# Kernel tuning notes

Hardware: AMD Instinct MI355X
Metric: run time of the kernel (lower is better)

## Reference

```python
import jax, jax.numpy as jnp
import numpy as np

TOP_K = 8
N_GROUPS = 8
TOP_K_GROUPS = 4
ROUTE_SCALE = 2.5


def setup_inputs() -> dict:
    key = jax.random.key(0)
    k1, k2, k3 = jax.random.split(key, 3)
    x = jax.random.normal(k1, (8192, 7168), dtype=jnp.float32)
    weight = jax.random.normal(k2, (256, 7168), dtype=jnp.float32) * 0.02
    bias = jax.random.normal(k3, (256,), dtype=jnp.float32) * 0.1
    return {"x": x, "weight": weight, "bias": bias}


def reference(x, weight, bias):
    n_tokens = x.shape[0]
    n_experts = weight.shape[0]
    # scores: [T, E]
    logits = jnp.einsum('td,ed->te', x, weight)
    scores = jax.nn.sigmoid(logits)
    original_scores = scores
    scores_b = scores + bias  # bias branch (dim == 7168)
    # group-limited routing
    sg = scores_b.reshape(n_tokens, N_GROUPS, n_experts // N_GROUPS)
    # bias is not None -> group score = sum of top-2 within group
    top2, _ = jax.lax.top_k(sg, 2)
    group_scores = top2.sum(axis=-1)  # [T, G]
    _, group_idx = jax.lax.top_k(group_scores, TOP_K_GROUPS)  # [T, Kg]
    keep = jnp.zeros((n_tokens, N_GROUPS), dtype=bool)
    keep = keep.at[jnp.arange(n_tokens)[:, None], group_idx].set(True)
    masked = jnp.where(keep[:, :, None], sg, -jnp.inf).reshape(n_tokens, n_experts)
    # global top-k over masked scores
    _, indices = jax.lax.top_k(masked, TOP_K)  # [T, K]
    weights = jnp.take_along_axis(original_scores, indices, axis=1)
    weights = weights / weights.sum(axis=-1, keepdims=True)  # sigmoid normalization
    weights = weights * ROUTE_SCALE
    return weights.astype(x.dtype), indices
```

## Files before the change

### kernel.cpp

```cpp
#include <hip/hip_runtime.h>
#include <math.h>

#define T_TOKENS 8192
#define NEXP 256
#define DIM 7168
#define NSPLIT 4
#define KSPL (DIM / NSPLIT)
#define NITER (KSPL / 32)
#define NEG_INF (-3.0e38f)

typedef _Float16 f16;
typedef _Float16 f16x8 __attribute__((ext_vector_type(8)));
typedef __fp16 h16x2 __attribute__((ext_vector_type(2)));
typedef float f32x4 __attribute__((ext_vector_type(4)));
typedef float f32x16 __attribute__((ext_vector_type(16)));

#define AS1 __attribute__((address_space(1)))
#define AS3 __attribute__((address_space(3)))
typedef const AS1 f16x8* gf16x8p;

#define WTILED_BYTES (2 * NEXP * DIM * 2)
#define PART_OFF WTILED_BYTES
#define UNSCALE 5.9604644775390625e-8f
#define STG 8192

__global__ __launch_bounds__(256) void wconvert(const float* __restrict__ w,
                                                char* __restrict__ wt) {
    const int n = blockIdx.x * 256 + threadIdx.x;
    const int K8 = n % 896;
    const int e = n / 896;
    const f32x4 u0 = *(const f32x4*)(w + (size_t)e * DIM + K8 * 8);
    const f32x4 u1 = *(const f32x4*)(w + (size_t)e * DIM + K8 * 8 + 4);
    float c[8] = {u0[0]*4096.f, u0[1]*4096.f, u0[2]*4096.f, u0[3]*4096.f,
                  u1[0]*4096.f, u1[1]*4096.f, u1[2]*4096.f, u1[3]*4096.f};
    f16x8 h, g;
#pragma unroll
    for (int j = 0; j < 4; ++j) {
        h16x2 hp = __builtin_amdgcn_cvt_pkrtz(c[2*j], c[2*j+1]);
        float r0 = c[2*j]   - (float)hp[0];
        float r1 = c[2*j+1] - (float)hp[1];
        h16x2 gp = __builtin_amdgcn_cvt_pkrtz(r0, r1);
        h[2*j] = (f16)hp[0]; h[2*j+1] = (f16)hp[1];
        g[2*j] = (f16)gp[0]; g[2*j+1] = (f16)gp[1];
    }
    const int T = K8 >> 2;
    const int kk = (K8 >> 1) & 1;
    const int lhi = K8 & 1;
    const int ntg = e >> 5, l31 = e & 31;
    char* base = wt + (size_t)T * 32768 + ntg * 1024 + lhi * 512 + l31 * 16;
    *(f16x8*)(base + (kk * 2 + 0) * 8192) = h;
    *(f16x8*)(base + (kk * 2 + 1) * 8192) = g;
}

__global__ __launch_bounds__(512, 4) void gemm_fo(
    const float* __restrict__ x, const char* __restrict__ wt,
    float* __restrict__ part) {
    __shared__ char smem[3 * STG];
    const int tid = threadIdx.x;
    const int lane = tid & 63;
    const int wcn = tid >> 6;
    const int b = blockIdx.x;
    const int xcd = b & 7;
    const int bz = xcd >> 1;
    const int bm = (xcd & 1) * 64 + (b >> 3);
    const int l31 = lane & 31, lhi = lane >> 5;

    const char* xc = (const char*)x;

    const int mt_s = wcn >> 2, kk_s = (wcn >> 1) & 1, j_s = wcn & 1;
    const int aoff = ((bm * 64 + mt_s * 32 + l31) * DIM + bz * KSPL
                      + kk_s * 16 + lhi * 8 + j_s * 4) * 4;
    const int ldsA = wcn * 1024;

    const AS1 char* wq = (const AS1 char*)(wt + (size_t)bz * NITER * 32768
                                           + wcn * 1024 + lane * 16);

    f32x16 acc[2];
#pragma unroll
    for (int mt = 0; mt < 2; ++mt)
#pragma unroll
        for (int r = 0; r < 16; ++r) acc[mt][r] = 0.0f;

    f16x8 wA[2][2], wB[2][2];

#define LOAD_W(T, WDST)                                                         \
    {                                                                           \
        _Pragma("unroll")                                                       \
        for (int kk = 0; kk < 2; ++kk)                                          \
            _Pragma("unroll")                                                   \
            for (int p = 0; p < 2; ++p)                                         \
                WDST[kk][p] = *(gf16x8p)(wq + (size_t)(T) * 32768 + (kk * 2 + p) * 8192); \
    }

#define COMPUTE(CB, W)                                                          \
    {                                                                           \
        _Pragma("unroll")                                                       \
        for (int kk = 0; kk < 2; ++kk) {                                        \
            _Pragma("unroll")                                                   \
            for (int mt = 0; mt < 2; ++mt) {                                    \
                const f32x4 v0 = *(const f32x4*)(smem + (CB) + (mt * 4 + kk * 2 + 0) * 1024 + lane * 16); \
                const f32x4 v1 = *(const f32x4*)(smem + (CB) + (mt * 4 + kk * 2 + 1) * 1024 + lane * 16); \
                float c[8] = {v0[0]*4096.f, v0[1]*4096.f, v0[2]*4096.f, v0[3]*4096.f,\
                              v1[0]*4096.f, v1[1]*4096.f, v1[2]*4096.f, v1[3]*4096.f};\
                f16x8 a0, a1;                                                   \
                _Pragma("unroll")                                               \
                for (int j = 0; j < 4; ++j) {                                   \
                    h16x2 hp = __builtin_amdgcn_cvt_pkrtz(c[2*j], c[2*j+1]);    \
                    float r0 = c[2*j]   - (float)hp[0];                         \
                    float r1 = c[2*j+1] - (float)hp[1];                         \
                    h16x2 gp = __builtin_amdgcn_cvt_pkrtz(r0, r1);              \
                    a0[2*j] = (f16)hp[0]; a0[2*j+1] = (f16)hp[1];               \
                    a1[2*j] = (f16)gp[0]; a1[2*j+1] = (f16)gp[1];               \
                }                                                               \
                __builtin_amdgcn_s_setprio(1);                                  \
                acc[mt] = __builtin_amdgcn_mfma_f32_32x32x16_f16(a0, W[kk][0], acc[mt], 0, 0, 0); \
                acc[mt] = __builtin_amdgcn_mfma_f32_32x32x16_f16(a1, W[kk][0], acc[mt], 0, 0, 0); \
                acc[mt] = __builtin_amdgcn_mfma_f32_32x32x16_f16(a0, W[kk][1], acc[mt], 0, 0, 0); \
                acc[mt] = __builtin_amdgcn_mfma_f32_32x32x16_f16(a1, W[kk][1], acc[mt], 0, 0, 0); \
                __builtin_amdgcn_s_setprio(0);                                  \
            }                                                                   \
        }                                                                       \
    }

#define BODY(T, WCUR, WNXT)                                                     \
    {                                                                           \
        asm volatile("s_waitcnt vmcnt(1)" ::: "memory");                        \
        __builtin_amdgcn_sched_barrier(0);                                      \
        __builtin_amdgcn_s_barrier();    \
        const int tw = ((T) + 1 < NITER) ? (T) + 1 : 0;                         \
        LOAD_W(tw, WNXT);                                                       \
        const int ts = ((T) + 2 < NITER) ? (T) + 2 : 0;                         \
        __builtin_amdgcn_global_load_lds(                                       \
            (const AS1 void*)(xc + aoff + ts * 128),                            \
            (AS3 void*)(smem + sb + ldsA), 16, 0, 0);                           \
        COMPUTE(cb, WCUR);                                                      \
        cb = (cb == 2 * STG) ? 0 : cb + STG;                                    \
        sb = (sb == 2 * STG) ? 0 : sb + STG;                                    \
    }

    __builtin_amdgcn_global_load_lds((const AS1 void*)(xc + aoff),
                                     (AS3 void*)(smem + ldsA), 16, 0, 0);
    LOAD_W(0, wA);
    __builtin_amdgcn_global_load_lds((const AS1 void*)(xc + aoff + 128),
                                     (AS3 void*)(smem + STG + ldsA), 16, 0, 0);

    int cb = 0, sb = 2 * STG;
    for (int tt = 0; tt < NITER; tt += 2) {
        BODY(tt, wA, wB);
        BODY(tt + 1, wB, wA);
    }
#undef BODY
#undef COMPUTE
#undef LOAD_W

    float* P = part + (size_t)bz * T_TOKENS * NEXP;
    const int gcol = wcn * 32 + l31;
#pragma unroll
    for (int mt = 0; mt < 2; ++mt)
#pragma unroll
        for (int r = 0; r < 16; ++r) {
            const int row32 = (r & 3) + 8 * (r >> 2) + 4 * lhi;
            const int grow = bm * 64 + mt * 32 + row32;
            P[(size_t)grow * NEXP + gcol] = acc[mt][r];
        }
}

__global__ __launch_bounds__(256) void routing_kernel(const float* __restrict__ part,
                                                      const float* __restrict__ bias,
                                                      float* __restrict__ out) {
    const int lane = threadIdx.x & 63;
    const int t = blockIdx.x * 4 + (threadIdx.x >> 6);

    f32x4 z = {0.f, 0.f, 0.f, 0.f};
#pragma unroll
    for (int s = 0; s < NSPLIT; ++s) {
        const f32x4 v = *((const f32x4*)(part + ((size_t)s * T_TOKENS + t) * NEXP) + lane);
        z[0] += v[0]; z[1] += v[1]; z[2] += v[2]; z[3] += v[3];
    }
    const float s0 = 1.0f / (1.0f + expf(-z[0] * UNSCALE));
    const float s1 = 1.0f / (1.0f + expf(-z[1] * UNSCALE));
    const float s2 = 1.0f / (1.0f + expf(-z[2] * UNSCALE));
    const float s3 = 1.0f / (1.0f + expf(-z[3] * UNSCALE));
    const f32x4 bv = *((const f32x4*)bias + lane);
    float sb0 = s0 + bv[0], sb1 = s1 + bv[1], sb2 = s2 + bv[2], sb3 = s3 + bv[3];

    float m1, m2;
    m1 = sb0; m2 = NEG_INF;
    if (sb1 > m1) { m2 = m1; m1 = sb1; } else if (sb1 > m2) m2 = sb1;
    if (sb2 > m1) { m2 = m1; m1 = sb2; } else if (sb2 > m2) m2 = sb2;
    if (sb3 > m1) { m2 = m1; m1 = sb3; } else if (sb3 > m2) m2 = sb3;
#pragma unroll
    for (int off = 1; off < 8; off <<= 1) {
        const float om1 = __shfl_xor(m1, off);
        const float om2 = __shfl_xor(m2, off);
        const float hi = fmaxf(m1, om1);
        const float lo = fminf(m1, om1);
        m2 = fmaxf(lo, fmaxf(m2, om2));
        m1 = hi;
    }
    const float gs = m1 + m2;

    const float g0 = __shfl(gs, 0),  g1 = __shfl(gs, 8),  g2 = __shfl(gs, 16), g3 = __shfl(gs, 24);
    const float g4 = __shfl(gs, 32), g5 = __shfl(gs, 40), g6 = __shfl(gs, 48), g7 = __shfl(gs, 56);

    float t1 = NEG_INF, t2 = NEG_INF, t3 = NEG_INF, t4 = NEG_INF;
    int i1 = 0, i2 = 0, i3 = 0, i4 = 0;
#define INS4(v, gi)                                                         \
    {                                                                       \
        if (v > t1)      { t4=t3;i4=i3; t3=t2;i3=i2; t2=t1;i2=i1; t1=v;i1=gi; } \
        else if (v > t2) { t4=t3;i4=i3; t3=t2;i3=i2; t2=v;i2=gi; }          \
        else if (v > t3) { t4=t3;i4=i3; t3=v;i3=gi; }                       \
        else if (v > t4) { t4=v;i4=gi; }                                    \
    }
    INS4(g0, 0) INS4(g1, 1) INS4(g2, 2) INS4(g3, 3)
    INS4(g4, 4) INS4(g5, 5) INS4(g6, 6) INS4(g7, 7)
#undef INS4
    const int keepmask = (1 << i1) | (1 << i2) | (1 << i3) | (1 << i4);

    const int g = lane >> 3;
    if (!((keepmask >> g) & 1)) { sb0 = NEG_INF; sb1 = NEG_INF; sb2 = NEG_INF; sb3 = NEG_INF; }

    float wval[8];
    int wi[8];
    float wsum = 0.0f;
#pragma unroll
    for (int r = 0; r < 8; r++) {
        float bvv = sb0;
        int bii = (lane << 2);
        if (sb1 > bvv) { bvv = sb1; bii = (lane << 2) | 1; }
        if (sb2 > bvv) { bvv = sb2; bii = (lane << 2) | 2; }
        if (sb3 > bvv) { bvv = sb3; bii = (lane << 2) | 3; }
#pragma unroll
        for (int off = 1; off < 64; off <<= 1) {
            const float ov = __shfl_xor(bvv, off);
            const int oi = __shfl_xor(bii, off);
            if (ov > bvv || (ov == bvv && oi < bii)) { bvv = ov; bii = oi; }
        }
        const int sl = bii & 3;
        const float cand = (sl == 0) ? s0 : (sl == 1) ? s1 : (sl == 2) ? s2 : s3;
        const float ow = __shfl(cand, bii >> 2);
        wval[r] = ow;
        wi[r] = bii;
        wsum += ow;
        if ((bii >> 2) == lane) {
            if (sl == 0) sb0 = NEG_INF;
            else if (sl == 1) sb1 = NEG_INF;
            else if (sl == 2) sb2 = NEG_INF;
            else sb3 = NEG_INF;
        }
    }
    const float scale = 2.5f / wsum;
    if (lane == 0) {
        float* ow8 = out + (size_t)t * 8;
        float* oi8 = out + (size_t)T_TOKENS * 8 + (size_t)t * 8;
#pragma unroll
        for (int r = 0; r < 8; r++) {
            ow8[r] = wval[r] * scale;
            oi8[r] = (float)wi[r];
        }
    }
}

extern "C" void kernel_launch(void* const* d_in, const int* in_sizes, int n_in,
                              void* d_out, int out_size, void* d_ws, size_t ws_size,
                              hipStream_t stream) {
    const float* x = (const float*)d_in[0];
    const float* w = (const float*)d_in[1];
    const float* bias = (const float*)d_in[2];

    char* wt = (char*)d_ws;
    float* part = (float*)((char*)d_ws + PART_OFF);

    wconvert<<<NEXP * DIM / (256 * 8), 256, 0, stream>>>(w, wt);
    gemm_fo<<<512, 512, 0, stream>>>(x, wt, part);
    routing_kernel<<<T_TOKENS / 4, 256, 0, stream>>>(part, bias, (float*)d_out);
}
```

Measured before the change: 169.8 us.

## Stage weight tiles through LDS and split waves over M and N

```diff
diff --git a/kernel.cpp b/kernel.cpp
--- a/kernel.cpp
+++ b/kernel.cpp
@@ -17,12 +17,11 @@
 
 #define AS1 __attribute__((address_space(1)))
 #define AS3 __attribute__((address_space(3)))
-typedef const AS1 f16x8* gf16x8p;
 
 #define WTILED_BYTES (2 * NEXP * DIM * 2)
 #define PART_OFF WTILED_BYTES
 #define UNSCALE 5.9604644775390625e-8f
-#define STG 8192
+#define STG 40960
 
 __global__ __launch_bounds__(256) void wconvert(const float* __restrict__ w,
                                                 char* __restrict__ wt) {
@@ -52,13 +51,14 @@
     *(f16x8*)(base + (kk * 2 + 1) * 8192) = g;
 }
 
-__global__ __launch_bounds__(512, 4) void gemm_fo(
+__global__ __launch_bounds__(512, 4) void gemm_bn(
     const float* __restrict__ x, const char* __restrict__ wt,
     float* __restrict__ part) {
-    __shared__ char smem[3 * STG];
+    extern __shared__ __align__(16) char smem[];
     const int tid = threadIdx.x;
     const int lane = tid & 63;
     const int wcn = tid >> 6;
+    const int wm = wcn >> 2, wn = wcn & 3;
     const int b = blockIdx.x;
     const int xcd = b & 7;
     const int bz = xcd >> 1;
@@ -71,98 +71,88 @@
     const int aoff = ((bm * 64 + mt_s * 32 + l31) * DIM + bz * KSPL
                       + kk_s * 16 + lhi * 8 + j_s * 4) * 4;
     const int ldsA = wcn * 1024;
-
-    const AS1 char* wq = (const AS1 char*)(wt + (size_t)bz * NITER * 32768
-                                           + wcn * 1024 + lane * 16);
+    const char* wsrc = wt + (size_t)bz * NITER * 32768;
+    const int woffb = wcn * 4096 + lane * 16;
+    const int ldsW = 8192 + wcn * 4096;
 
     f32x16 acc[2];
 #pragma unroll
-    for (int mt = 0; mt < 2; ++mt)
-#pragma unroll
-        for (int r = 0; r < 16; ++r) acc[mt][r] = 0.0f;
-
-    f16x8 wA[2][2], wB[2][2];
-
-#define LOAD_W(T, WDST)                                                         \
+    for (int ntl = 0; ntl < 2; ++ntl)
+#pragma unroll
+        for (int r = 0; r < 16; ++r) acc[ntl][r] = 0.0f;
+
+#define STAGE(T, SB)                                                            \
     {                                                                           \
+        __builtin_amdgcn_global_load_lds(                                       \
+            (const AS1 void*)(xc + aoff + (T) * 128),                           \
+            (AS3 void*)(smem + (SB) + ldsA), 16, 0, 0);                         \
         _Pragma("unroll")                                                       \
-        for (int kk = 0; kk < 2; ++kk)                                          \
-            _Pragma("unroll")                                                   \
-            for (int p = 0; p < 2; ++p)                                         \
-                WDST[kk][p] = *(gf16x8p)(wq + (size_t)(T) * 32768 + (kk * 2 + p) * 8192); \
-    }
-
-#define COMPUTE(CB, W)                                                          \
+        for (int i = 0; i < 4; ++i)                                             \
+            __builtin_amdgcn_global_load_lds(                                   \
+                (const AS1 void*)(wsrc + (size_t)(T) * 32768 + woffb + i * 1024),\
+                (AS3 void*)(smem + (SB) + ldsW + i * 1024), 16, 0, 0);          \
+    }
+
+#define COMPUTE(CB)                                                             \
     {                                                                           \
         _Pragma("unroll")                                                       \
         for (int kk = 0; kk < 2; ++kk) {                                        \
+            const f32x4 v0 = *(const f32x4*)(smem + (CB) + (wm * 4 + kk * 2 + 0) * 1024 + lane * 16); \
+            const f32x4 v1 = *(const f32x4*)(smem + (CB) + (wm * 4 + kk * 2 + 1) * 1024 + lane * 16); \
+            float c[8] = {v0[0]*4096.f, v0[1]*4096.f, v0[2]*4096.f, v0[3]*4096.f,\
+                          v1[0]*4096.f, v1[1]*4096.f, v1[2]*4096.f, v1[3]*4096.f};\
+            f16x8 a0, a1;                                                       \
             _Pragma("unroll")                                                   \
-            for (int mt = 0; mt < 2; ++mt) {                                    \
-                const f32x4 v0 = *(const f32x4*)(smem + (CB) + (mt * 4 + kk * 2 + 0) * 1024 + lane * 16); \
-                const f32x4 v1 = *(const f32x4*)(smem + (CB) + (mt * 4 + kk * 2 + 1) * 1024 + lane * 16); \
-                float c[8] = {v0[0]*4096.f, v0[1]*4096.f, v0[2]*4096.f, v0[3]*4096.f,\
-                              v1[0]*4096.f, v1[1]*4096.f, v1[2]*4096.f, v1[3]*4096.f};\
-                f16x8 a0, a1;                                                   \
+            for (int j = 0; j < 4; ++j) {                                       \
+                h16x2 hp = __builtin_amdgcn_cvt_pkrtz(c[2*j], c[2*j+1]);        \
+                float r0 = c[2*j]   - (float)hp[0];                             \
+                float r1 = c[2*j+1] - (float)hp[1];                             \
+                h16x2 gp = __builtin_amdgcn_cvt_pkrtz(r0, r1);                  \
+                a0[2*j] = (f16)hp[0]; a0[2*j+1] = (f16)hp[1];                   \
+                a1[2*j] = (f16)gp[0]; a1[2*j+1] = (f16)gp[1];                   \
+            }                                                                   \
+            f16x8 wb[2][2];                                                     \
+            _Pragma("unroll")                                                   \
+            for (int p = 0; p < 2; ++p)                                         \
                 _Pragma("unroll")                                               \
-                for (int j = 0; j < 4; ++j) {                                   \
-                    h16x2 hp = __builtin_amdgcn_cvt_pkrtz(c[2*j], c[2*j+1]);    \
-                    float r0 = c[2*j]   - (float)hp[0];                         \
-                    float r1 = c[2*j+1] - (float)hp[1];                         \
-                    h16x2 gp = __builtin_amdgcn_cvt_pkrtz(r0, r1);              \
-                    a0[2*j] = (f16)hp[0]; a0[2*j+1] = (f16)hp[1];               \
-                    a1[2*j] = (f16)gp[0]; a1[2*j+1] = (f16)gp[1];               \
-                }                                                               \
-                __builtin_amdgcn_s_setprio(1);                                  \
-                acc[mt] = __builtin_amdgcn_mfma_f32_32x32x16_f16(a0, W[kk][0], acc[mt], 0, 0, 0); \
-                acc[mt] = __builtin_amdgcn_mfma_f32_32x32x16_f16(a1, W[kk][0], acc[mt], 0, 0, 0); \
-                acc[mt] = __builtin_amdgcn_mfma_f32_32x32x16_f16(a0, W[kk][1], acc[mt], 0, 0, 0); \
-                acc[mt] = __builtin_amdgcn_mfma_f32_32x32x16_f16(a1, W[kk][1], acc[mt], 0, 0, 0); \
-                __builtin_amdgcn_s_setprio(0);                                  \
+                for (int ntl = 0; ntl < 2; ++ntl)                               \
+                    wb[p][ntl] = *(const f16x8*)(smem + (CB) + 8192             \
+                        + ((kk * 2 + p) * 8 + wn * 2 + ntl) * 1024 + lane * 16);\
+            __builtin_amdgcn_s_setprio(1);                                      \
+            _Pragma("unroll")                                                   \
+            for (int ntl = 0; ntl < 2; ++ntl) {                                 \
+                acc[ntl] = __builtin_amdgcn_mfma_f32_32x32x16_f16(a0, wb[0][ntl], acc[ntl], 0, 0, 0); \
+                acc[ntl] = __builtin_amdgcn_mfma_f32_32x32x16_f16(a1, wb[0][ntl], acc[ntl], 0, 0, 0); \
+                acc[ntl] = __builtin_amdgcn_mfma_f32_32x32x16_f16(a0, wb[1][ntl], acc[ntl], 0, 0, 0); \
+                acc[ntl] = __builtin_amdgcn_mfma_f32_32x32x16_f16(a1, wb[1][ntl], acc[ntl], 0, 0, 0); \
             }                                                                   \
+            __builtin_amdgcn_s_setprio(0);                                      \
         }                                                                       \
     }
 
-#define BODY(T, WCUR, WNXT)                                                     \
-    {                                                                           \
-        asm volatile("s_waitcnt vmcnt(1)" ::: "memory");                        \
-        __builtin_amdgcn_sched_barrier(0);                                      \
-        __builtin_amdgcn_s_barrier();    \
-        const int tw = ((T) + 1 < NITER) ? (T) + 1 : 0;                         \
-        LOAD_W(tw, WNXT);                                                       \
-        const int ts = ((T) + 2 < NITER) ? (T) + 2 : 0;                         \
-        __builtin_amdgcn_global_load_lds(                                       \
-            (const AS1 void*)(xc + aoff + ts * 128),                            \
-            (AS3 void*)(smem + sb + ldsA), 16, 0, 0);                           \
-        COMPUTE(cb, WCUR);                                                      \
-        cb = (cb == 2 * STG) ? 0 : cb + STG;                                    \
-        sb = (sb == 2 * STG) ? 0 : sb + STG;                                    \
-    }
-
-    __builtin_amdgcn_global_load_lds((const AS1 void*)(xc + aoff),
-                                     (AS3 void*)(smem + ldsA), 16, 0, 0);
-    LOAD_W(0, wA);
-    __builtin_amdgcn_global_load_lds((const AS1 void*)(xc + aoff + 128),
-                                     (AS3 void*)(smem + STG + ldsA), 16, 0, 0);
-
-    int cb = 0, sb = 2 * STG;
-    for (int tt = 0; tt < NITER; tt += 2) {
-        BODY(tt, wA, wB);
-        BODY(tt + 1, wB, wA);
-    }
-#undef BODY
+    STAGE(0, 0);
+    for (int t = 0; t < NITER; ++t) {
+        asm volatile("s_waitcnt vmcnt(0)" ::: "memory");
+        __builtin_amdgcn_sched_barrier(0);
+        __builtin_amdgcn_s_barrier();
+        const int tn = (t + 1 < NITER) ? t + 1 : 0;
+        STAGE(tn, ((t + 1) & 1) * STG);
+        COMPUTE((t & 1) * STG);
+    }
+#undef STAGE
 #undef COMPUTE
-#undef LOAD_W
 
     float* P = part + (size_t)bz * T_TOKENS * NEXP;
-    const int gcol = wcn * 32 + l31;
-#pragma unroll
-    for (int mt = 0; mt < 2; ++mt)
+#pragma unroll
+    for (int ntl = 0; ntl < 2; ++ntl) {
+        const int gcol = wn * 64 + ntl * 32 + l31;
 #pragma unroll
         for (int r = 0; r < 16; ++r) {
             const int row32 = (r & 3) + 8 * (r >> 2) + 4 * lhi;
-            const int grow = bm * 64 + mt * 32 + row32;
-            P[(size_t)grow * NEXP + gcol] = acc[mt][r];
-        }
+            const int grow = bm * 64 + wm * 32 + row32;
+            P[(size_t)grow * NEXP + gcol] = acc[ntl][r];
+        }
+    }
 }
 
 __global__ __launch_bounds__(256) void routing_kernel(const float* __restrict__ part,
@@ -271,7 +261,10 @@
     char* wt = (char*)d_ws;
     float* part = (float*)((char*)d_ws + PART_OFF);
 
+    (void)hipFuncSetAttribute((const void*)gemm_bn,
+                              hipFuncAttributeMaxDynamicSharedMemorySize, 2 * STG);
+
     wconvert<<<NEXP * DIM / (256 * 8), 256, 0, stream>>>(w, wt);
-    gemm_fo<<<512, 512, 0, stream>>>(x, wt, part);
+    gemm_bn<<<512, 512, 2 * STG, stream>>>(x, wt, part);
     routing_kernel<<<T_TOKENS / 4, 256, 0, stream>>>(part, bias, (float*)d_out);
 }
```

Result: faster. 163.1 us (-3.9%).
